# Optimization experiments

Hardware: AMD Instinct MI355X
Metric: run time of the kernel (lower is better)

The kernel has to match this reference:

```python
import jax, jax.numpy as jnp
import numpy as np
from jax import lax


def setup_inputs() -> dict:
    key = jax.random.key(0)
    k1, k2 = jax.random.split(key)
    B, C, H, W = 4, 64, 64, 64
    foreground = jax.random.normal(k1, (B, C, H, W), dtype=jnp.float32)
    masks = jax.random.uniform(k2, (B, 1, H, W), dtype=jnp.float32)
    return {"foreground": foreground, "masks": masks}


def reference(foreground, masks):
    # First-call path of KnowledgeConsistentAttention (att_scores_prev is None).
    # patch_size=3 -> padding=1 around 1x1 dynamic kernels; propagate_size=3 -> 3x3 sum pool.
    B, C, H, W = foreground.shape
    P = H * W
    # Dynamic 1x1 kernels: one per spatial location, L2-normalized over channels.
    K = foreground.reshape(B, C, P).transpose(0, 2, 1)            # [B, P, C]
    norm = jnp.sqrt(jnp.sum(K * K, axis=2, keepdims=True))        # flatten(1).norm per kernel
    K = K / (norm + 1e-8)
    # conv2d with 1x1 kernels and padding=1 == GEMM over zero-padded input.
    Xpad = jnp.pad(foreground, ((0, 0), (0, 0), (1, 1), (1, 1)))  # [B, C, H+2, W+2]
    scores = jnp.einsum('bpc,bchw->bphw', K, Xpad)                # [B, P, H+2, W+2]
    # avg_pool2d(k=3, stride=1, pad=1) * 9 == zero-padded 3x3 sum pool.
    scores = lax.reduce_window(scores, jnp.float32(0.0), lax.add,
                               (1, 1, 3, 3), (1, 1, 1, 1), 'SAME')
    attn = jax.nn.softmax(scores, axis=1)                          # softmax over P kernels
    # conv_transpose2d with 1x1 kernels, padding=1 crops the border back to HxW.
    out = jnp.einsum('bphw,bpc->bchw', attn[:, :, 1:-1, 1:-1], K)  # [B, C, H, W]
    return out
```

## Files before the change

kernel.cpp:

```cpp
#include <hip/hip_runtime.h>
#include <hip/hip_bf16.h>
#include <math.h>

#define Bn 4
#define Cn 64
#define Pn 4096
#define QT 64
#define PBK 128
#define NITER (Pn / PBK)
#define LOG2E 1.4426950408889634f

typedef __attribute__((ext_vector_type(8))) short short8;
typedef __attribute__((ext_vector_type(4))) short short4v;
typedef __attribute__((ext_vector_type(4))) float float4v;
typedef unsigned short bfu;

__device__ __forceinline__ bfu f2bf(float x) {
    unsigned u = __float_as_uint(x);
    u = (u + 0x7fffu + ((u >> 16) & 1u)) >> 16;
    return (bfu)u;
}

__device__ __forceinline__ void async_load16(const bfu* g, bfu* l) {
    __builtin_amdgcn_global_load_lds(
        (const __attribute__((address_space(1))) unsigned int*)(const void*)g,
        (__attribute__((address_space(3))) unsigned int*)(void*)l,
        16, 0, 0);
}

__global__ __launch_bounds__(256) void prep_kernel(const float* __restrict__ fg,
                                                   bfu* __restrict__ Kpc,
                                                   bfu* __restrict__ Kcp2,
                                                   float* __restrict__ S) {
    __shared__ float shbuf[64 * 64];
    int t = threadIdx.x;
    if (blockIdx.x < 512) {
        float* tile  = shbuf;
        float* rnorm = shbuf + 64 * 33;
        int b  = blockIdx.x >> 7;
        int p0 = (blockIdx.x & 127) << 5;
        const float* src = fg + (size_t)b * Cn * Pn + p0;
        #pragma unroll
        for (int i = 0; i < 8; ++i) {
            int idx = i * 256 + t;
            int c = idx >> 5, p = idx & 31;
            tile[c * 33 + p] = src[(size_t)c * Pn + p];
        }
        __syncthreads();
        if (t < 32) {
            float ss = 0.f;
            #pragma unroll
            for (int c = 0; c < 64; ++c) { float v = tile[c * 33 + t]; ss += v * v; }
            rnorm[t] = 1.0f / (sqrtf(ss) + 1e-8f);
        }
        __syncthreads();
        bfu* dpc = Kpc + ((size_t)b * Pn + p0) * Cn;
        #pragma unroll
        for (int i = 0; i < 8; ++i) {
            int idx = i * 256 + t;
            int p = idx >> 6, c = idx & 63;
            dpc[(size_t)p * Cn + c] = f2bf(tile[c * 33 + p] * rnorm[p]);
        }
        bfu* d2 = Kcp2 + ((size_t)b * 256 + (p0 >> 4)) * 1024;
        #pragma unroll
        for (int i = 0; i < 8; ++i) {
            int idx = i * 256 + t;
            int c = idx >> 5, p = idx & 31;
            d2[(size_t)(p >> 4) * 1024 + c * 16 + (p & 15)] =
                f2bf(tile[c * 33 + p] * rnorm[p]);
        }
    } else {
        float (*pl)[64] = (float(*)[64])shbuf;
        int bc = blockIdx.x - 512;
        const float* src = fg + (size_t)bc * Pn;
        float*       dst = S  + (size_t)bc * Pn;
        #pragma unroll
        for (int i = 0; i < 16; ++i) {
            int idx = i * 256 + t;
            pl[idx >> 6][idx & 63] = src[idx];
        }
        __syncthreads();
        #pragma unroll
        for (int i = 0; i < 16; ++i) {
            int idx = i * 256 + t;
            int h = idx >> 6, w = idx & 63;
            float s = 0.f;
            #pragma unroll
            for (int dh = -1; dh <= 1; ++dh) {
                int hh = h + dh;
                if (hh < 0 || hh >= 64) continue;
                #pragma unroll
                for (int dw = -1; dw <= 1; ++dw) {
                    int ww = w + dw;
                    if (ww < 0 || ww >= 64) continue;
                    s += pl[hh][ww];
                }
            }
            dst[idx] = s * LOG2E;
        }
    }
}

__global__ __launch_bounds__(512, 1) void flash_kernel(const bfu* __restrict__ Kpc,
                                                       const bfu* __restrict__ Kcp2,
                                                       const float* __restrict__ S,
                                                       float* __restrict__ out) {
    __shared__ __align__(16) bfu smem[33792];
    __shared__ float wredl[8][QT];
    bfu* Sl = smem + 16384;

    int i  = blockIdx.x;
    int b  = (i & 7) >> 1;
    int qt = ((i >> 3) << 1) | (i & 1);
    int q0 = qt * QT;
    int t  = threadIdx.x;
    int w = t >> 6, l = t & 63, lq = l & 15, quad = l >> 4;

    const float* Sg  = S    + (size_t)b * Cn * Pn;
    const bfu*   gpc = Kpc  + (size_t)b * Pn * Cn;
    const bfu*   gt  = Kcp2 + (size_t)b * 256 * 1024;

    {
        int c = t >> 3, qq = (t & 7) * 8;
        const float* sp = &Sg[(size_t)c * Pn + q0 + qq];
        float4 v0 = *(const float4*)sp;
        float4 v1 = *(const float4*)(sp + 4);
        float vv[8] = {v0.x, v0.y, v0.z, v0.w, v1.x, v1.y, v1.z, v1.w};
        int ch = c >> 3, cl = c & 7;
        #pragma unroll
        for (int k = 0; k < 8; ++k) {
            int row = qq + k;
            Sl[row * 64 + ((ch ^ (row & 7)) << 3) + cl] = f2bf(vv[k]);
        }
    }

    {
        const bfu* src = gt + (size_t)w * 1024 + l * 8;
        bfu* dst = smem + w * 1024;
        async_load16(src, dst);
        async_load16(src + 512, dst + 512);
    }
    __syncthreads();

    short8 bs[4][2];
    #pragma unroll
    for (int nt = 0; nt < 4; ++nt)
        #pragma unroll
        for (int ks = 0; ks < 2; ++ks) {
            int row = nt * 16 + lq;
            bs[nt][ks] = *(const short8*)&Sl[row * 64 + (((ks * 4 + quad) ^ (lq & 7)) << 3)];
        }

    float4v o[4][4];
    #pragma unroll
    for (int nt = 0; nt < 4; ++nt)
        #pragma unroll
        for (int cb = 0; cb < 4; ++cb) o[nt][cb] = (float4v){0.f, 0.f, 0.f, 0.f};
    float lacc[4] = {0.f, 0.f, 0.f, 0.f};

    for (int pb = 0; pb < NITER; ++pb) {
        bfu* tile = smem + (pb & 1) * 8192 + w * 1024;

        const bfu* ap = gpc + ((size_t)pb * PBK + 16 * w + lq) * Cn + quad * 8;
        float4 a0 = *(const float4*)ap;
        float4 a1 = *(const float4*)(ap + 32);

        if (pb + 1 < NITER) {
            const bfu* src = gt + ((size_t)(pb + 1) * 8 + w) * 1024 + l * 8;
            bfu* dst = smem + ((pb + 1) & 1) * 8192 + w * 1024;
            async_load16(src, dst);
            async_load16(src + 512, dst + 512);
        }

        short8 af0 = *(short8*)&a0, af1 = *(short8*)&a1;
        float4v sc[4];
        #pragma unroll
        for (int nt = 0; nt < 4; ++nt) {
            float4v acc = (float4v){0.f, 0.f, 0.f, 0.f};
            acc = __builtin_amdgcn_mfma_f32_16x16x32_bf16(af0, bs[nt][0], acc, 0, 0, 0);
            acc = __builtin_amdgcn_mfma_f32_16x16x32_bf16(af1, bs[nt][1], acc, 0, 0, 0);
            sc[nt] = acc;
        }

        short4v epk[4];
        #pragma unroll
        for (int nt = 0; nt < 4; ++nt) {
            float e0 = __builtin_amdgcn_exp2f(sc[nt][0]);
            float e1 = __builtin_amdgcn_exp2f(sc[nt][1]);
            float e2 = __builtin_amdgcn_exp2f(sc[nt][2]);
            float e3 = __builtin_amdgcn_exp2f(sc[nt][3]);
            lacc[nt] += (e0 + e1) + (e2 + e3);
            short4v ep = {(short)f2bf(e0), (short)f2bf(e1), (short)f2bf(e2), (short)f2bf(e3)};
            epk[nt] = ep;
        }

        __builtin_amdgcn_s_waitcnt(0x0F72);
        __builtin_amdgcn_sched_barrier(0);

        #pragma unroll
        for (int cb = 0; cb < 4; ++cb) {
            short4v kb = *(const short4v*)&tile[(16 * cb + lq) * 16 + quad * 4];
            #pragma unroll
            for (int nt = 0; nt < 4; ++nt)
                o[nt][cb] = __builtin_amdgcn_mfma_f32_16x16x16bf16_1k(epk[nt], kb, o[nt][cb], 0, 0, 0);
        }
    }

    #pragma unroll
    for (int nt = 0; nt < 4; ++nt) {
        lacc[nt] += __shfl_xor(lacc[nt], 16);
        lacc[nt] += __shfl_xor(lacc[nt], 32);
    }
    if (quad == 0)
        #pragma unroll
        for (int nt = 0; nt < 4; ++nt) wredl[w][nt * 16 + lq] = lacc[nt];

    float* Ol = (float*)smem;
    __syncthreads();
    if (w < 4) {
        #pragma unroll
        for (int nt = 0; nt < 4; ++nt)
            #pragma unroll
            for (int cb = 0; cb < 4; ++cb)
                #pragma unroll
                for (int r = 0; r < 4; ++r)
                    Ol[(w * 64 + 16 * cb + lq) * 66 + nt * 16 + quad * 4 + r] = o[nt][cb][r];
    }
    __syncthreads();
    if (w >= 4) {
        #pragma unroll
        for (int nt = 0; nt < 4; ++nt)
            #pragma unroll
            for (int cb = 0; cb < 4; ++cb)
                #pragma unroll
                for (int r = 0; r < 4; ++r)
                    Ol[((w - 4) * 64 + 16 * cb + lq) * 66 + nt * 16 + quad * 4 + r] += o[nt][cb][r];
    }
    __syncthreads();

    float* og = out + (size_t)b * Cn * Pn;
    #pragma unroll
    for (int k = 0; k < 8; ++k) {
        int idx = k * 512 + t;
        int c = idx >> 6, q = idx & 63;
        float lsum = ((wredl[0][q] + wredl[1][q]) + (wredl[2][q] + wredl[3][q])) +
                     ((wredl[4][q] + wredl[5][q]) + (wredl[6][q] + wredl[7][q]));
        float v = ((Ol[c * 66 + q] + Ol[(64 + c) * 66 + q]) +
                   (Ol[(128 + c) * 66 + q] + Ol[(192 + c) * 66 + q])) / lsum;
        og[(size_t)c * Pn + q0 + q] = v;
    }
}

extern "C" void kernel_launch(void* const* d_in, const int* in_sizes, int n_in,
                              void* d_out, int out_size, void* d_ws, size_t ws_size,
                              hipStream_t stream) {
    const float* fg = (const float*)d_in[0];
    float* out = (float*)d_out;
    bfu*   Kpc  = (bfu*)d_ws;
    bfu*   Kcp2 = Kpc + (size_t)Bn * Pn * Cn;
    float* S    = (float*)(Kcp2 + (size_t)Bn * Pn * Cn);

    prep_kernel <<<768, 256, 0, stream>>>(fg, Kpc, Kcp2, S);
    flash_kernel<<<Bn * 64, 512, 0, stream>>>(Kpc, Kcp2, S, out);
}
```

Baseline: 95.98 us.

## Replace LDS async double-buffer with register-prefetched direct global loads

```diff
diff --git a/kernel.cpp b/kernel.cpp
--- a/kernel.cpp
+++ b/kernel.cpp
@@ -19,13 +19,6 @@
     unsigned u = __float_as_uint(x);
     u = (u + 0x7fffu + ((u >> 16) & 1u)) >> 16;
     return (bfu)u;
-}
-
-__device__ __forceinline__ void async_load16(const bfu* g, bfu* l) {
-    __builtin_amdgcn_global_load_lds(
-        (const __attribute__((address_space(1))) unsigned int*)(const void*)g,
-        (__attribute__((address_space(3))) unsigned int*)(void*)l,
-        16, 0, 0);
 }
 
 __global__ __launch_bounds__(256) void prep_kernel(const float* __restrict__ fg,
@@ -107,7 +100,7 @@
                                                        float* __restrict__ out) {
     __shared__ __align__(16) bfu smem[33792];
     __shared__ float wredl[8][QT];
-    bfu* Sl = smem + 16384;
+    bfu* Sl = smem;
 
     int i  = blockIdx.x;
     int b  = (i & 7) >> 1;
@@ -133,13 +126,6 @@
             Sl[row * 64 + ((ch ^ (row & 7)) << 3) + cl] = f2bf(vv[k]);
         }
     }
-
-    {
-        const bfu* src = gt + (size_t)w * 1024 + l * 8;
-        bfu* dst = smem + w * 1024;
-        async_load16(src, dst);
-        async_load16(src + 512, dst + 512);
-    }
     __syncthreads();
 
     short8 bs[4][2];
@@ -158,18 +144,25 @@
         for (int cb = 0; cb < 4; ++cb) o[nt][cb] = (float4v){0.f, 0.f, 0.f, 0.f};
     float lacc[4] = {0.f, 0.f, 0.f, 0.f};
 
+    const bfu* ap = gpc + ((size_t)16 * w + lq) * Cn + quad * 8;
+    const bfu* tp = gt + (size_t)w * 1024 + lq * 16 + quad * 4;
+
+    float4 a0 = *(const float4*)ap;
+    float4 a1 = *(const float4*)(ap + 32);
+    short4v kb[4];
+    #pragma unroll
+    for (int cb = 0; cb < 4; ++cb) kb[cb] = *(const short4v*)(tp + cb * 256);
+
     for (int pb = 0; pb < NITER; ++pb) {
-        bfu* tile = smem + (pb & 1) * 8192 + w * 1024;
-
-        const bfu* ap = gpc + ((size_t)pb * PBK + 16 * w + lq) * Cn + quad * 8;
-        float4 a0 = *(const float4*)ap;
-        float4 a1 = *(const float4*)(ap + 32);
-
+        float4 na0, na1;
+        short4v nkb[4];
         if (pb + 1 < NITER) {
-            const bfu* src = gt + ((size_t)(pb + 1) * 8 + w) * 1024 + l * 8;
-            bfu* dst = smem + ((pb + 1) & 1) * 8192 + w * 1024;
-            async_load16(src, dst);
-            async_load16(src + 512, dst + 512);
+            const bfu* apn = ap + (size_t)(pb + 1) * PBK * Cn;
+            na0 = *(const float4*)apn;
+            na1 = *(const float4*)(apn + 32);
+            const bfu* tpn = tp + (size_t)(pb + 1) * 8 * 1024;
+            #pragma unroll
+            for (int cb = 0; cb < 4; ++cb) nkb[cb] = *(const short4v*)(tpn + cb * 256);
         }
 
         short8 af0 = *(short8*)&a0, af1 = *(short8*)&a1;
@@ -194,16 +187,16 @@
             epk[nt] = ep;
         }
 
-        __builtin_amdgcn_s_waitcnt(0x0F72);
-        __builtin_amdgcn_sched_barrier(0);
-
         #pragma unroll
         for (int cb = 0; cb < 4; ++cb) {
-            short4v kb = *(const short4v*)&tile[(16 * cb + lq) * 16 + quad * 4];
             #pragma unroll
             for (int nt = 0; nt < 4; ++nt)
-                o[nt][cb] = __builtin_amdgcn_mfma_f32_16x16x16bf16_1k(epk[nt], kb, o[nt][cb], 0, 0, 0);
-        }
+                o[nt][cb] = __builtin_amdgcn_mfma_f32_16x16x16bf16_1k(epk[nt], kb[cb], o[nt][cb], 0, 0, 0);
+        }
+
+        a0 = na0; a1 = na1;
+        #pragma unroll
+        for (int cb = 0; cb < 4; ++cb) kb[cb] = nkb[cb];
     }
 
     #pragma unroll
```

Result: faster. 92.42 us, median of 2 (-3.7%).

## Pack K operands in MFMA fragment order and triple-buffer async LDS loads

Applied to the files above, without the earlier changes.

```diff
diff --git a/kernel.cpp b/kernel.cpp
--- a/kernel.cpp
+++ b/kernel.cpp
@@ -29,8 +29,7 @@
 }
 
 __global__ __launch_bounds__(256) void prep_kernel(const float* __restrict__ fg,
-                                                   bfu* __restrict__ Kpc,
-                                                   bfu* __restrict__ Kcp2,
+                                                   bfu* __restrict__ KOP,
                                                    float* __restrict__ S) {
     __shared__ float shbuf[64 * 64];
     int t = threadIdx.x;
@@ -54,20 +53,27 @@
             rnorm[t] = 1.0f / (sqrtf(ss) + 1e-8f);
         }
         __syncthreads();
-        bfu* dpc = Kpc + ((size_t)b * Pn + p0) * Cn;
-        #pragma unroll
-        for (int i = 0; i < 8; ++i) {
-            int idx = i * 256 + t;
-            int p = idx >> 6, c = idx & 63;
-            dpc[(size_t)p * Cn + c] = f2bf(tile[c * 33 + p] * rnorm[p]);
-        }
-        bfu* d2 = Kcp2 + ((size_t)b * 256 + (p0 >> 4)) * 1024;
-        #pragma unroll
-        for (int i = 0; i < 8; ++i) {
-            int idx = i * 256 + t;
-            int c = idx >> 5, p = idx & 31;
-            d2[(size_t)(p >> 4) * 1024 + c * 16 + (p & 15)] =
-                f2bf(tile[c * 33 + p] * rnorm[p]);
+        int r = t >> 6, l = t & 63, lq = l & 15, quad = l >> 4;
+        #pragma unroll
+        for (int h = 0; h < 2; ++h) {
+            bfu v[8];
+            if (r == 0 || r == 1) {
+                int p = 16 * h + lq;
+                float rn = rnorm[p];
+                #pragma unroll
+                for (int m = 0; m < 8; ++m)
+                    v[m] = f2bf(tile[(r * 32 + quad * 8 + m) * 33 + p] * rn);
+            } else {
+                #pragma unroll
+                for (int m = 0; m < 8; ++m) {
+                    int u = (r - 2) * 2 + (m >> 2), i = m & 3;
+                    int p = 16 * h + quad * 4 + i;
+                    v[m] = f2bf(tile[(16 * u + lq) * 33 + p] * rnorm[p]);
+                }
+            }
+            bfu* dst = KOP + ((size_t)(b * 256 + (p0 >> 4) + h)) * 2048 + t * 8;
+            *(ushort4*)dst       = make_ushort4(v[0], v[1], v[2], v[3]);
+            *(ushort4*)(dst + 4) = make_ushort4(v[4], v[5], v[6], v[7]);
         }
     } else {
         float (*pl)[64] = (float(*)[64])shbuf;
@@ -101,13 +107,12 @@
     }
 }
 
-__global__ __launch_bounds__(512, 1) void flash_kernel(const bfu* __restrict__ Kpc,
-                                                       const bfu* __restrict__ Kcp2,
+__global__ __launch_bounds__(512, 1) void flash_kernel(const bfu* __restrict__ KOP,
                                                        const float* __restrict__ S,
                                                        float* __restrict__ out) {
-    __shared__ __align__(16) bfu smem[33792];
+    __shared__ __align__(16) bfu smem[53248];
     __shared__ float wredl[8][QT];
-    bfu* Sl = smem + 16384;
+    bfu* Sl = smem + 49152;
 
     int i  = blockIdx.x;
     int b  = (i & 7) >> 1;
@@ -116,9 +121,8 @@
     int t  = threadIdx.x;
     int w = t >> 6, l = t & 63, lq = l & 15, quad = l >> 4;
 
-    const float* Sg  = S    + (size_t)b * Cn * Pn;
-    const bfu*   gpc = Kpc  + (size_t)b * Pn * Cn;
-    const bfu*   gt  = Kcp2 + (size_t)b * 256 * 1024;
+    const float* Sg  = S   + (size_t)b * Cn * Pn;
+    const bfu*   gop = KOP + (size_t)b * 256 * 2048;
 
     {
         int c = t >> 3, qq = (t & 7) * 8;
@@ -134,11 +138,14 @@
         }
     }
 
-    {
-        const bfu* src = gt + (size_t)w * 1024 + l * 8;
-        bfu* dst = smem + w * 1024;
-        async_load16(src, dst);
-        async_load16(src + 512, dst + 512);
+    bfu* obuf = smem + w * 6144;
+
+    #pragma unroll
+    for (int s = 0; s < 2; ++s) {
+        const bfu* src = gop + (size_t)(s * 8 + w) * 2048 + l * 8;
+        #pragma unroll
+        for (int R = 0; R < 4; ++R)
+            async_load16(src + R * 512, obuf + s * 2048 + R * 512);
     }
     __syncthreads();
 
@@ -159,20 +166,29 @@
     float lacc[4] = {0.f, 0.f, 0.f, 0.f};
 
     for (int pb = 0; pb < NITER; ++pb) {
-        bfu* tile = smem + (pb & 1) * 8192 + w * 1024;
-
-        const bfu* ap = gpc + ((size_t)pb * PBK + 16 * w + lq) * Cn + quad * 8;
-        float4 a0 = *(const float4*)ap;
-        float4 a1 = *(const float4*)(ap + 32);
-
-        if (pb + 1 < NITER) {
-            const bfu* src = gt + ((size_t)(pb + 1) * 8 + w) * 1024 + l * 8;
-            bfu* dst = smem + ((pb + 1) & 1) * 8192 + w * 1024;
-            async_load16(src, dst);
-            async_load16(src + 512, dst + 512);
-        }
-
-        short8 af0 = *(short8*)&a0, af1 = *(short8*)&a1;
+        if (pb + 2 < NITER) {
+            int sn = (pb + 2) % 3;
+            const bfu* src = gop + (size_t)((pb + 2) * 8 + w) * 2048 + l * 8;
+            #pragma unroll
+            for (int R = 0; R < 4; ++R)
+                async_load16(src + R * 512, obuf + sn * 2048 + R * 512);
+        }
+
+        __builtin_amdgcn_sched_barrier(0);
+        __builtin_amdgcn_s_waitcnt(0x0F78);
+        __builtin_amdgcn_sched_barrier(0);
+
+        bfu* slot = obuf + (pb % 3) * 2048;
+        short8 af0 = *(const short8*)(slot + l * 8);
+        short8 af1 = *(const short8*)(slot + 512 + l * 8);
+        short8 b01 = *(const short8*)(slot + 1024 + l * 8);
+        short8 b23 = *(const short8*)(slot + 1536 + l * 8);
+        short4v kb[4];
+        kb[0] = __builtin_shufflevector(b01, b01, 0, 1, 2, 3);
+        kb[1] = __builtin_shufflevector(b01, b01, 4, 5, 6, 7);
+        kb[2] = __builtin_shufflevector(b23, b23, 0, 1, 2, 3);
+        kb[3] = __builtin_shufflevector(b23, b23, 4, 5, 6, 7);
+
         float4v sc[4];
         #pragma unroll
         for (int nt = 0; nt < 4; ++nt) {
@@ -194,15 +210,11 @@
             epk[nt] = ep;
         }
 
-        __builtin_amdgcn_s_waitcnt(0x0F72);
-        __builtin_amdgcn_sched_barrier(0);
-
         #pragma unroll
         for (int cb = 0; cb < 4; ++cb) {
-            short4v kb = *(const short4v*)&tile[(16 * cb + lq) * 16 + quad * 4];
             #pragma unroll
             for (int nt = 0; nt < 4; ++nt)
-                o[nt][cb] = __builtin_amdgcn_mfma_f32_16x16x16bf16_1k(epk[nt], kb, o[nt][cb], 0, 0, 0);
+                o[nt][cb] = __builtin_amdgcn_mfma_f32_16x16x16bf16_1k(epk[nt], kb[cb], o[nt][cb], 0, 0, 0);
         }
     }
 
@@ -256,10 +268,9 @@
                               hipStream_t stream) {
     const float* fg = (const float*)d_in[0];
     float* out = (float*)d_out;
-    bfu*   Kpc  = (bfu*)d_ws;
-    bfu*   Kcp2 = Kpc + (size_t)Bn * Pn * Cn;
-    float* S    = (float*)(Kcp2 + (size_t)Bn * Pn * Cn);
-
-    prep_kernel <<<768, 256, 0, stream>>>(fg, Kpc, Kcp2, S);
-    flash_kernel<<<Bn * 64, 512, 0, stream>>>(Kpc, Kcp2, S, out);
-}
+    bfu*   KOP = (bfu*)d_ws;
+    float* S   = (float*)(KOP + (size_t)Bn * 256 * 2048);
+
+    prep_kernel <<<768, 256, 0, stream>>>(fg, KOP, S);
+    flash_kernel<<<Bn * 64, 512, 0, stream>>>(KOP, S, out);
+}
```

Measured after the change: 95.67 us. Within noise of the previous version (-0.3%).
